# Kernel optimization log

Measured on AMD Instinct MI355X. Metric: run time of the kernel, lower is better.

## Reference

```python
import jax, jax.numpy as jnp
import numpy as np

S = 30000      # num sessions (= num clicks)
ND = 300000    # num displayed rows (10 per session)
F = 64         # f_dim
I = 500        # item_size (news_cnt_short)
PW = 10        # pw_dim
BAND = 20      # pw_band_size
H = 256        # mlp hidden


def setup_inputs() -> dict:
    key = jax.random.key(0)
    ks = jax.random.split(key, 8)
    per = ND // S  # disp rows per session
    disp_sec = jnp.repeat(jnp.arange(S, dtype=jnp.int64), per)          # sorted, every segment nonempty
    click_sub = jnp.arange(S, dtype=jnp.int64) * per                     # one clicked disp row per session
    # banded lower-triangular cumulative-sum indices: row r attends to cols r-0..r-(BAND-1) (clipped at 0)
    rows = jnp.repeat(jnp.arange(S, dtype=jnp.int64), BAND)
    offs = jnp.tile(jnp.arange(BAND, dtype=jnp.int64), S)
    cols = jnp.clip(rows - offs, 0)
    tril_idx = jnp.stack([rows, cols], axis=1)                            # [NT,2]
    click_items = jax.random.randint(ks[0], (S,), 0, I, dtype=jnp.int64)
    disp_items = jax.random.randint(ks[1], (ND,), 0, I, dtype=jnp.int64)
    return {
        'disp_current_feature': jax.random.normal(ks[2], (ND, F), dtype=jnp.float32),
        'Xs_clicked': jax.random.normal(ks[3], (S, F), dtype=jnp.float32),
        'W1': jax.random.normal(ks[4], (F * PW + F, H), dtype=jnp.float32) * 0.05,
        'b1': jnp.zeros((H,), jnp.float32),
        'W2': jax.random.normal(ks[5], (H, H), dtype=jnp.float32) * 0.05,
        'b2': jnp.zeros((H,), jnp.float32),
        'W3': jax.random.normal(ks[6], (H, 1), dtype=jnp.float32) * 0.05,
        'b3': jnp.zeros((1,), jnp.float32),
        'cumsum_tril_indices': tril_idx,
        'cumsum_tril_value_indices': offs,
        'disp_2d_split_sec_ind': disp_sec,
        'click_2d_subindex': click_sub,
        'click_indices': jnp.stack([jnp.arange(S, dtype=jnp.int64), click_items], axis=1),
        'disp_indices': jnp.stack([disp_sec, disp_items], axis=1),
        'section_length': S,
        'item_size': I,
        'pw_dim': PW,
        'band_size': BAND,
    }


def reference(disp_current_feature, Xs_clicked, W1, b1, W2, b2, W3, b3,
              cumsum_tril_indices, cumsum_tril_value_indices,
              disp_2d_split_sec_ind, click_2d_subindex,
              click_indices, disp_indices,
              section_length, item_size, pw_dim, band_size):
    # position weights (fixed 1e-4 as in original forward), gathered per sparse entry
    position_weight = jnp.full((band_size,), 1e-4, dtype=jnp.float32)
    vals = position_weight[cumsum_tril_value_indices]                     # [NT]
    # sparse [S,S] matmul with Xs_clicked expressed as gather + segment_sum (same math as dense matmul)
    contrib = vals[:, None] * Xs_clicked[cumsum_tril_indices[:, 1]]       # [NT,F]
    hist = jax.ops.segment_sum(contrib, cumsum_tril_indices[:, 0], num_segments=section_length)  # [S,F]
    # the pw_dim copies are identical (same position_weight each loop iteration)
    concat_history = jnp.concatenate([hist] * pw_dim, axis=1)             # [S, PW*F]
    disp_hist = concat_history[disp_2d_split_sec_ind]                     # [ND, PW*F]
    feats = jnp.concatenate([disp_hist, disp_current_feature], axis=1)    # [ND, (PW+1)*F]
    h = jax.nn.elu(feats @ W1 + b1)
    h = jax.nn.elu(h @ W2 + b2)
    u_disp = h @ W3 + b3                                                  # [ND,1]
    exp_u = jnp.exp(u_disp)
    sum_exp = jax.ops.segment_sum(exp_u, disp_2d_split_sec_ind, num_segments=section_length)  # [S,1]
    sum_click_u = u_disp[click_2d_subindex]                               # [S,1]
    loss_sum = jnp.sum(-sum_click_u + jnp.log(sum_exp + 1.0))
    click_tensor = jnp.zeros((section_length, item_size), jnp.float32).at[
        click_indices[:, 0], click_indices[:, 1]].add(1.0)
    event_cnt = jnp.sum(click_tensor)
    loss = loss_sum / event_cnt
    dense_exp = jnp.zeros((section_length, item_size), jnp.float32).at[
        disp_indices[:, 0], disp_indices[:, 1]].add(exp_u[:, 0])
    argmax_click = jnp.argmax(click_tensor, axis=1)
    argmax_disp = jnp.argmax(dense_exp, axis=1)
    top2 = jax.lax.top_k(dense_exp, 2)[1]                                 # [S,2]
    p1_sum = jnp.sum(argmax_click == argmax_disp)
    p2_sum = jnp.sum(argmax_click[:, None] == top2)
    precision_1 = p1_sum / event_cnt
    precision_2 = p2_sum / event_cnt
    return (loss, precision_1, precision_2, loss_sum, p1_sum, p2_sum, event_cnt)
```

## Files before the change

kernel.cpp:

```cpp
#include <hip/hip_runtime.h>
#include <hip/hip_bf16.h>

#define TPB 256

typedef _Float16 f16;
typedef f16 f16x8 __attribute__((ext_vector_type(8)));
typedef f16 f16x4 __attribute__((ext_vector_type(4)));
typedef f16 f16x2 __attribute__((ext_vector_type(2)));
typedef float f32x16 __attribute__((ext_vector_type(16)));
typedef unsigned int uint;

union F16x8U { f16x8 v; uint4 q; };
union F16x4U { f16x4 v; uint2 q; };

__device__ __forceinline__ float elu_f(float z) {
    return z > 0.f ? z : __expf(z) - 1.f;
}

__global__ void prepw0_kernel(const float* __restrict__ W1, int PW,
                              f16* __restrict__ W1sT_hi) {
    int t = blockIdx.x * blockDim.x + threadIdx.x;
    if (t < 16384) {
        int n = t >> 6, k = t & 63;
        float s = 0.f;
        for (int p = 0; p < PW; ++p) s += W1[(size_t)(p * 64 + k) * 256 + n];
        W1sT_hi[t] = (f16)s;
    }
}

__global__ __launch_bounds__(TPB, 2) void hist_ahist_kernel(
    const float* __restrict__ Xs, const int* __restrict__ tril,
    const f16* __restrict__ W1sT_hi, const float* __restrict__ b1,
    f16* __restrict__ Ah16, int S, int band,
    const float* __restrict__ W1, const float* __restrict__ W2, int PW,
    f16* __restrict__ W1bT_hi, f16* __restrict__ W2sw,
    int HB)
{
    __shared__ float wA[147 * 68];
    __shared__ f16  hB[128 * 72];

    const int tid = threadIdx.x;

    if ((int)blockIdx.x >= HB) {
        int t = (blockIdx.x - HB) * TPB + tid;
        if (t < 16384) {
            int n = t >> 6, k = t & 63;
            W1bT_hi[t] = (f16)W1[(size_t)(PW * 64 + k) * 256 + n];
        } else {
            int t2 = t - 16384;
            int e  = t2 & 7;
            int n  = (t2 >> 3) & 255;
            int kh = t2 >> 11;
            int k  = (kh >> 1) * 16 + (kh & 1) * 8 + e;
            W2sw[t2] = (f16)W2[(size_t)k * 256 + n];
        }
        return;
    }

    const int SB = blockIdx.x * 128;
    const int base = SB >= 19 ? SB - 19 : 0;

    for (int i = tid; i < 147 * 16; i += TPB) {
        int row = i >> 4, q = i & 15;
        int src = base + row; if (src > S - 1) src = S - 1;
        float4 v = *(const float4*)&Xs[(size_t)src * 64 + q * 4];
        *(float4*)&wA[row * 68 + q * 4] = v;
    }
    __syncthreads();

    const int f = tid & 63, w = tid >> 6;
    for (int k = 0; k < 32; ++k) {
        int rl = w * 32 + k;
        int rg = SB + rl; if (rg > S - 1) rg = S - 1;
        const int* tre = tril + (size_t)rg * band * 2;
        float acc = 0.f;
        for (int o = 0; o < band; ++o) {
            int c = tre[o * 2 + 1] - base;
            c = c < 0 ? 0 : (c > 146 ? 146 : c);
            acc += wA[c * 68 + f];
        }
        hB[rl * 72 + f] = (f16)(acc * 1e-4f);
    }
    __syncthreads();

    const int l = tid & 63, lr = l & 31, hh = l >> 5;
    const int nt0 = 2 * w;

    #pragma unroll
    for (int st = 0; st < 4; ++st) {
        int sgl = st * 32 + lr;
        F16x8U Bh[4];
        #pragma unroll
        for (int ks = 0; ks < 4; ++ks)
            Bh[ks].q = *(const uint4*)&hB[sgl * 72 + ks * 16 + 8 * hh];
        int sg = SB + sgl;
        #pragma unroll
        for (int jn = 0; jn < 2; ++jn) {
            int nt = nt0 + jn;
            f32x16 acc;
            #pragma unroll
            for (int rq = 0; rq < 4; ++rq) {
                float4 bq = *(const float4*)&b1[nt * 32 + rq * 8 + 4 * hh];
                acc[rq * 4 + 0] = bq.x; acc[rq * 4 + 1] = bq.y;
                acc[rq * 4 + 2] = bq.z; acc[rq * 4 + 3] = bq.w;
            }
            const f16* ah = W1sT_hi + (size_t)(nt * 32 + lr) * 64 + 8 * hh;
            #pragma unroll
            for (int ks = 0; ks < 4; ++ks) {
                f16x8 Ah = *(const f16x8*)(ah + ks * 16);
                acc = __builtin_amdgcn_mfma_f32_32x32x16_f16(Ah, Bh[ks].v, acc, 0, 0, 0);
            }
            if (sg < S) {
                F16x8U o0, o1;
                #pragma unroll
                for (int i = 0; i < 8; ++i) {
                    o0.v[i] = (f16)acc[i];
                    o1.v[i] = (f16)acc[8 + i];
                }
                f16* op = Ah16 + (((size_t)sg * 8 + nt) * 2 + hh) * 16;
                *(uint4*)op = o0.q;
                *(uint4*)(op + 8) = o1.q;
            }
        }
    }
}

__global__ __launch_bounds__(512, 4) void mlp14_kernel(
    const float* __restrict__ dispF, const f16* __restrict__ Ah16,
    const f16* __restrict__ W1bT_hi,
    const f16* __restrict__ W2sw,
    const float* __restrict__ b2, const float* __restrict__ W3,
    const float* __restrict__ b3, float* __restrict__ u,
    int ND, int per, float inv_per)
{
    __shared__ uint4 frag[4][16][64];
    f16* dstage = (f16*)&frag[3][0][0];

    const int tid = threadIdx.x;
    const int w = tid >> 6, l = tid & 63, lr = l & 31, hh = l >> 5;
    const int RB = blockIdx.x * 128;
    const int nt = w;

    #pragma unroll
    for (int r = 0; r < 4; ++r) {
        int i = r * 512 + tid;
        int row = i >> 4, q = i & 15;
        int k8 = q >> 1;
        int rg = RB + row; if (rg > ND - 1) rg = ND - 1;
        float4 v = *(const float4*)&dispF[(size_t)rg * 64 + q * 4];
        F16x4U o;
        o.v[0] = (f16)v.x; o.v[1] = (f16)v.y; o.v[2] = (f16)v.z; o.v[3] = (f16)v.w;
        *(uint2*)&dstage[(size_t)(((row >> 5) * 8 + k8) * 256)
                         + ((row & 31) ^ k8) * 8 + (q & 1) * 4] = o.q;
    }

    const f16* a1h = W1bT_hi + (size_t)(nt * 32 + lr) * 64 + 8 * hh;
    f16x8 A1h[4];
    #pragma unroll
    for (int ks = 0; ks < 4; ++ks) A1h[ks] = *(const f16x8*)(a1h + ks * 16);

    const f16* w2p = W2sw + (size_t)hh * 2048 + (size_t)(nt * 32 + lr) * 8;
    f16x8 W2p[4];
    #pragma unroll
    for (int kp = 0; kp < 4; ++kp) W2p[kp] = *(const f16x8*)(w2p + (size_t)kp * 4096);

    int srow[4];
    #pragma unroll
    for (int st = 0; st < 4; ++st) {
        int rg = RB + st * 32 + lr;
        int rgc = rg <= ND - 1 ? rg : ND - 1;
        int sr = (int)((float)rgc * inv_per);
        sr += ((sr + 1) * per <= rgc) ? 1 : 0;
        srow[st] = sr;
    }

    __syncthreads();

    f16x8 Db[2][4];
    uint4 AhP[2][2];
    #pragma unroll
    for (int b = 0; b < 2; ++b) {
        #pragma unroll
        for (int ks = 0; ks < 4; ++ks) {
            int k8 = ks * 2 + hh;
            Db[b][ks] = *(const f16x8*)&dstage[(size_t)((b * 8 + k8) * 256) + (lr ^ k8) * 8];
        }
        const f16* ap = Ah16 + (((size_t)srow[b] * 8 + nt) * 2 + hh) * 16;
        AhP[b][0] = *(const uint4*)ap;
        AhP[b][1] = *(const uint4*)(ap + 8);
    }

    #pragma unroll
    for (int st = 0; st < 4; ++st) {
        f32x16 acc;
        {
            F16x8U u0, u1; u0.q = AhP[st & 1][0]; u1.q = AhP[st & 1][1];
            #pragma unroll
            for (int i = 0; i < 8; ++i) {
                acc[i] = (float)u0.v[i];
                acc[8 + i] = (float)u1.v[i];
            }
        }
        if (st + 2 < 4) {
            const f16* ap = Ah16 + (((size_t)srow[st + 2] * 8 + nt) * 2 + hh) * 16;
            AhP[st & 1][0] = *(const uint4*)ap;
            AhP[st & 1][1] = *(const uint4*)(ap + 8);
        }
        #pragma unroll
        for (int ks = 0; ks < 4; ++ks) {
            acc = __builtin_amdgcn_mfma_f32_32x32x16_f16(A1h[ks], Db[st & 1][ks], acc, 0, 0, 0);
        }
        if (st + 2 < 4) {
            #pragma unroll
            for (int ks = 0; ks < 4; ++ks) {
                int k8 = ks * 2 + hh;
                Db[st & 1][ks] = *(const f16x8*)&dstage[
                    (size_t)(((st + 2) * 8 + k8) * 256) + (lr ^ k8) * 8];
            }
        }

        uint p[4][2];
        #pragma unroll
        for (int rq = 0; rq < 4; ++rq) {
            #pragma unroll
            for (int jj = 0; jj < 2; ++jj) {
                float a = elu_f(acc[rq * 4 + 2 * jj]);
                float b = elu_f(acc[rq * 4 + 2 * jj + 1]);
                f16x2 hp; hp[0] = (f16)a; hp[1] = (f16)b;
                p[rq][jj] = __builtin_bit_cast(uint, hp);
            }
        }
        #pragma unroll
        for (int c = 0; c < 2; ++c) {
            uint s0 = hh ? p[2 * c][0] : p[2 * c + 1][0];
            uint s1 = hh ? p[2 * c][1] : p[2 * c + 1][1];
            uint r0 = __shfl_xor(s0, 32, 64);
            uint r1 = __shfl_xor(s1, 32, 64);
            uint4 B;
            B.x = hh ? r0 : p[2 * c][0];
            B.y = hh ? r1 : p[2 * c][1];
            B.z = hh ? p[2 * c + 1][0] : r0;
            B.w = hh ? p[2 * c + 1][1] : r1;
            frag[st][2 * nt + c][l] = B;
        }
        if (st == 1) __syncthreads();
    }
    __syncthreads();

    f32x16 acc2[4];
    #pragma unroll
    for (int rq = 0; rq < 4; ++rq) {
        float4 bq = *(const float4*)&b2[nt * 32 + rq * 8 + 4 * hh];
        #pragma unroll
        for (int st = 0; st < 4; ++st) {
            acc2[st][rq * 4 + 0] = bq.x; acc2[st][rq * 4 + 1] = bq.y;
            acc2[st][rq * 4 + 2] = bq.z; acc2[st][rq * 4 + 3] = bq.w;
        }
    }

    #pragma unroll
    for (int kt = 0; kt < 16; ++kt) {
        f16x8 Ah = W2p[kt & 3];
        if (kt + 4 < 16) W2p[kt & 3] = *(const f16x8*)(w2p + (size_t)(kt + 4) * 4096);
        #pragma unroll
        for (int st = 0; st < 4; ++st) {
            F16x8U B; B.q = frag[st][kt][l];
            acc2[st] = __builtin_amdgcn_mfma_f32_32x32x16_f16(Ah, B.v, acc2[st], 0, 0, 0);
        }
    }

    float up[4] = {0.f, 0.f, 0.f, 0.f};
    #pragma unroll
    for (int rq = 0; rq < 4; ++rq) {
        float4 wq = *(const float4*)&W3[nt * 32 + rq * 8 + 4 * hh];
        #pragma unroll
        for (int st = 0; st < 4; ++st) {
            up[st] += elu_f(acc2[st][rq * 4 + 0]) * wq.x
                    + elu_f(acc2[st][rq * 4 + 1]) * wq.y
                    + elu_f(acc2[st][rq * 4 + 2]) * wq.z
                    + elu_f(acc2[st][rq * 4 + 3]) * wq.w;
        }
    }
    #pragma unroll
    for (int st = 0; st < 4; ++st) up[st] += __shfl_xor(up[st], 32, 64);

    __syncthreads();
    float* pb = (float*)frag;
    if (hh == 0) {
        #pragma unroll
        for (int st = 0; st < 4; ++st) pb[(w * 4 + st) * 32 + lr] = up[st];
    }
    __syncthreads();
    if (tid < 128) {
        int st = tid >> 5, lrr = tid & 31;
        float v = 0.f;
        #pragma unroll
        for (int w2 = 0; w2 < 8; ++w2) v += pb[(w2 * 4 + st) * 32 + lrr];
        int rg = RB + tid;
        if (rg < ND) u[rg] = v + b3[0];
    }
}

template <int PER>
__global__ void session_kernel(const float* __restrict__ u, const int* __restrict__ clickSub,
                               const int* __restrict__ clickIdx, const int* __restrict__ dispIdx,
                               float* __restrict__ pLoss, int* __restrict__ pP1,
                               int* __restrict__ pP2, int S) {
    int s = blockIdx.x * 64 + threadIdx.x;
    float lossv = 0.f; int p1 = 0, p2 = 0;
    if (s < S) {
        int base = s * PER;
        float ev[PER]; int it[PER];
        float sum_exp = 0.f;
        #pragma unroll
        for (int i = 0; i < PER; ++i) {
            float uu = u[base + i];
            ev[i] = expf(uu);
            sum_exp += ev[i];
            it[i] = dispIdx[(size_t)(base + i) * 2 + 1];
        }
        int crow = clickSub[s];
        lossv = -u[crow] + logf(sum_exp + 1.f);

        float bestv = -1.f; int besti = 0x7FFFFFFF;
        float secv = -1.f;  int seci = 0x7FFFFFFF;
        int ndist = 0;
        #pragma unroll
        for (int i = 0; i < PER; ++i) {
            bool first = true; float tot = 0.f;
            #pragma unroll
            for (int j = 0; j < PER; ++j) {
                if (it[j] == it[i]) { tot += ev[j]; if (j < i) first = false; }
            }
            if (first) {
                ndist++;
                if (tot > bestv || (tot == bestv && it[i] < besti)) {
                    secv = bestv; seci = besti;
                    bestv = tot;  besti = it[i];
                } else if (tot > secv || (tot == secv && it[i] < seci)) {
                    secv = tot; seci = it[i];
                }
            }
        }
        if (ndist < 2) seci = (besti == 0) ? 1 : 0;
        int citem = clickIdx[s * 2 + 1];
        p1 = (citem == besti) ? 1 : 0;
        p2 = (citem == besti || citem == seci) ? 1 : 0;
    }
    #pragma unroll
    for (int off = 32; off > 0; off >>= 1) {
        lossv += __shfl_xor(lossv, off, 64);
        p1 += __shfl_xor(p1, off, 64);
        p2 += __shfl_xor(p2, off, 64);
    }
    if (threadIdx.x == 0) {
        pLoss[blockIdx.x] = lossv; pP1[blockIdx.x] = p1; pP2[blockIdx.x] = p2;
    }
}

__global__ void finalize_kernel(const float* __restrict__ pLoss, const int* __restrict__ pP1,
                                const int* __restrict__ pP2, int nb, float event_cnt,
                                float* __restrict__ out) {
    __shared__ float sf[TPB]; __shared__ int s1[TPB]; __shared__ int s2[TPB];
    int t = threadIdx.x;
    float lf = 0.f; int a1 = 0, a2 = 0;
    for (int i = t; i < nb; i += TPB) { lf += pLoss[i]; a1 += pP1[i]; a2 += pP2[i]; }
    sf[t] = lf; s1[t] = a1; s2[t] = a2;
    __syncthreads();
    for (int off = TPB / 2; off > 0; off >>= 1) {
        if (t < off) { sf[t] += sf[t + off]; s1[t] += s1[t + off]; s2[t] += s2[t + off]; }
        __syncthreads();
    }
    if (t == 0) {
        float ls = sf[0];
        float p1 = (float)s1[0];
        float p2 = (float)s2[0];
        out[0] = ls / event_cnt;
        out[1] = p1 / event_cnt;
        out[2] = p2 / event_cnt;
        out[3] = ls;
        out[4] = p1;
        out[5] = p2;
        out[6] = event_cnt;
    }
}

extern "C" void kernel_launch(void* const* d_in, const int* in_sizes, int n_in,
                              void* d_out, int out_size, void* d_ws, size_t ws_size,
                              hipStream_t stream) {
    const float* dispF    = (const float*)d_in[0];
    const float* Xs       = (const float*)d_in[1];
    const float* W1       = (const float*)d_in[2];
    const float* b1       = (const float*)d_in[3];
    const float* W2       = (const float*)d_in[4];
    const float* b2       = (const float*)d_in[5];
    const float* W3       = (const float*)d_in[6];
    const float* b3       = (const float*)d_in[7];
    const int*   tril     = (const int*)d_in[8];
    const int*   clickSub = (const int*)d_in[11];
    const int*   clickIdx = (const int*)d_in[12];
    const int*   dispIdx  = (const int*)d_in[13];

    const int S    = in_sizes[11];
    const int ND   = in_sizes[10];
    const int F    = in_sizes[1] / S;
    const int H    = in_sizes[3];
    const int NT   = in_sizes[9];
    const int BAND = NT / S;
    const int PW   = in_sizes[2] / (F * H) - 1;
    const int per  = ND / S;

    const int nblk = (ND + 127) / 128;
    const int HB   = (S + 127) / 128;

    float* ws    = (float*)d_ws;
    float* u     = ws;
    const int nb5 = (S + 63) / 64;
    float* pLoss = u + ((size_t)ND + 128);
    int*   pP1   = (int*)(pLoss + nb5);
    int*   pP2   = pP1 + nb5;
    size_t f32_used = (size_t)(pP2 + nb5 - (int*)ws);
    f32_used = (f32_used + 3) & ~(size_t)3;
    f16* W1bT_hi = (f16*)(ws + f32_used);
    f16* W1sT_hi = W1bT_hi + 16384;
    f16* W2sw    = W1sT_hi + 16384;
    f16* Ah16    = W2sw + 65536;

    prepw0_kernel<<<64, TPB, 0, stream>>>(W1, PW, W1sT_hi);
    hist_ahist_kernel<<<HB + 320, TPB, 0, stream>>>(
        Xs, tril, W1sT_hi, b1, Ah16, S, BAND,
        W1, W2, PW, W1bT_hi, W2sw, HB);
    mlp14_kernel<<<nblk, 512, 0, stream>>>(
        dispF, Ah16, W1bT_hi, W2sw, b2, W3, b3, u,
        ND, per, 1.0f / (float)per);
    session_kernel<10><<<nb5, 64, 0, stream>>>(u, clickSub, clickIdx, dispIdx, pLoss, pP1, pP2, S);
    finalize_kernel<<<1, TPB, 0, stream>>>(pLoss, pP1, pP2, nb5, (float)S, (float*)d_out);
}
```

Measured before the change: 143.1 us.

## Split W2 MFMA into two halves, coalesce weight prep writes, vectorize session loads

The layer-2 MFMA loop now processes two sub-tiles at a time in a non-unrolled loop with two accumulators instead of four. This cuts accumulator register pressure, and W2 prefetch wraps around for the second half. Weight-prep kernels now iterate with n fastest so the fp32 W1/W2 reads are coalesced, while the f16 stores become strided. The session kernel loads u and dispIdx with float2/int4 vector loads. The trade-off is serialized MFMA halves with less interleaving, plus reloading W2 fragments for the second half.

```diff
diff --git a/kernel.cpp b/kernel.cpp
--- a/kernel.cpp
+++ b/kernel.cpp
@@ -21,10 +21,10 @@
                               f16* __restrict__ W1sT_hi) {
     int t = blockIdx.x * blockDim.x + threadIdx.x;
     if (t < 16384) {
-        int n = t >> 6, k = t & 63;
+        int k = t >> 8, n = t & 255;
         float s = 0.f;
         for (int p = 0; p < PW; ++p) s += W1[(size_t)(p * 64 + k) * 256 + n];
-        W1sT_hi[t] = (f16)s;
+        W1sT_hi[n * 64 + k] = (f16)s;
     }
 }
 
@@ -44,15 +44,12 @@
     if ((int)blockIdx.x >= HB) {
         int t = (blockIdx.x - HB) * TPB + tid;
         if (t < 16384) {
-            int n = t >> 6, k = t & 63;
-            W1bT_hi[t] = (f16)W1[(size_t)(PW * 64 + k) * 256 + n];
+            int k = t >> 8, n = t & 255;
+            W1bT_hi[n * 64 + k] = (f16)W1[(size_t)(PW * 64 + k) * 256 + n];
         } else {
             int t2 = t - 16384;
-            int e  = t2 & 7;
-            int n  = (t2 >> 3) & 255;
-            int kh = t2 >> 11;
-            int k  = (kh >> 1) * 16 + (kh & 1) * 8 + e;
-            W2sw[t2] = (f16)W2[(size_t)k * 256 + n];
+            int k = t2 >> 8, n = t2 & 255;
+            W2sw[(size_t)(k >> 3) * 2048 + n * 8 + (k & 7)] = (f16)W2[(size_t)k * 256 + n];
         }
         return;
     }
@@ -125,7 +122,7 @@
     }
 }
 
-__global__ __launch_bounds__(512, 4) void mlp14_kernel(
+__global__ __launch_bounds__(512, 4) void mlp15_kernel(
     const float* __restrict__ dispF, const f16* __restrict__ Ah16,
     const f16* __restrict__ W1bT_hi,
     const f16* __restrict__ W2sw,
@@ -247,40 +244,47 @@
     }
     __syncthreads();
 
-    f32x16 acc2[4];
-    #pragma unroll
-    for (int rq = 0; rq < 4; ++rq) {
-        float4 bq = *(const float4*)&b2[nt * 32 + rq * 8 + 4 * hh];
-        #pragma unroll
-        for (int st = 0; st < 4; ++st) {
-            acc2[st][rq * 4 + 0] = bq.x; acc2[st][rq * 4 + 1] = bq.y;
-            acc2[st][rq * 4 + 2] = bq.z; acc2[st][rq * 4 + 3] = bq.w;
-        }
-    }
-
-    #pragma unroll
-    for (int kt = 0; kt < 16; ++kt) {
-        f16x8 Ah = W2p[kt & 3];
-        if (kt + 4 < 16) W2p[kt & 3] = *(const f16x8*)(w2p + (size_t)(kt + 4) * 4096);
-        #pragma unroll
-        for (int st = 0; st < 4; ++st) {
-            F16x8U B; B.q = frag[st][kt][l];
-            acc2[st] = __builtin_amdgcn_mfma_f32_32x32x16_f16(Ah, B.v, acc2[st], 0, 0, 0);
-        }
-    }
-
-    float up[4] = {0.f, 0.f, 0.f, 0.f};
-    #pragma unroll
-    for (int rq = 0; rq < 4; ++rq) {
-        float4 wq = *(const float4*)&W3[nt * 32 + rq * 8 + 4 * hh];
-        #pragma unroll
-        for (int st = 0; st < 4; ++st) {
-            up[st] += elu_f(acc2[st][rq * 4 + 0]) * wq.x
-                    + elu_f(acc2[st][rq * 4 + 1]) * wq.y
-                    + elu_f(acc2[st][rq * 4 + 2]) * wq.z
-                    + elu_f(acc2[st][rq * 4 + 3]) * wq.w;
-        }
-    }
+    float4 bq2 = *(const float4*)&b2[nt * 32 + 0 * 8 + 4 * hh];
+    float up[4];
+
+    #pragma unroll 1
+    for (int half = 0; half < 2; ++half) {
+        const int s0i = 2 * half, s1i = 2 * half + 1;
+        f32x16 accA, accB;
+        #pragma unroll
+        for (int rq = 0; rq < 4; ++rq) {
+            float4 bq = *(const float4*)&b2[nt * 32 + rq * 8 + 4 * hh];
+            accA[rq * 4 + 0] = bq.x; accA[rq * 4 + 1] = bq.y;
+            accA[rq * 4 + 2] = bq.z; accA[rq * 4 + 3] = bq.w;
+            accB[rq * 4 + 0] = bq.x; accB[rq * 4 + 1] = bq.y;
+            accB[rq * 4 + 2] = bq.z; accB[rq * 4 + 3] = bq.w;
+        }
+        #pragma unroll
+        for (int kt = 0; kt < 16; ++kt) {
+            f16x8 Ah = W2p[kt & 3];
+            if (kt + 4 < 16) {
+                W2p[kt & 3] = *(const f16x8*)(w2p + (size_t)(kt + 4) * 4096);
+            } else if (half == 0) {
+                W2p[kt & 3] = *(const f16x8*)(w2p + (size_t)(kt - 12) * 4096);
+            }
+            F16x8U BA; BA.q = frag[s0i][kt][l];
+            F16x8U BB; BB.q = frag[s1i][kt][l];
+            accA = __builtin_amdgcn_mfma_f32_32x32x16_f16(Ah, BA.v, accA, 0, 0, 0);
+            accB = __builtin_amdgcn_mfma_f32_32x32x16_f16(Ah, BB.v, accB, 0, 0, 0);
+        }
+        float uA = 0.f, uB = 0.f;
+        #pragma unroll
+        for (int rq = 0; rq < 4; ++rq) {
+            float4 wq = *(const float4*)&W3[nt * 32 + rq * 8 + 4 * hh];
+            uA += elu_f(accA[rq * 4 + 0]) * wq.x + elu_f(accA[rq * 4 + 1]) * wq.y
+                + elu_f(accA[rq * 4 + 2]) * wq.z + elu_f(accA[rq * 4 + 3]) * wq.w;
+            uB += elu_f(accB[rq * 4 + 0]) * wq.x + elu_f(accB[rq * 4 + 1]) * wq.y
+                + elu_f(accB[rq * 4 + 2]) * wq.z + elu_f(accB[rq * 4 + 3]) * wq.w;
+        }
+        up[s0i] = uA; up[s1i] = uB;
+    }
+    (void)bq2;
+
     #pragma unroll
     for (int st = 0; st < 4; ++st) up[st] += __shfl_xor(up[st], 32, 64);
 
@@ -309,15 +313,22 @@
     int s = blockIdx.x * 64 + threadIdx.x;
     float lossv = 0.f; int p1 = 0, p2 = 0;
     if (s < S) {
-        int base = s * PER;
         float ev[PER]; int it[PER];
+        const float2* up2 = (const float2*)(u + (size_t)s * PER);
+        const int4* dp4 = (const int4*)(dispIdx + (size_t)s * PER * 2);
+        float uu[PER];
+        #pragma unroll
+        for (int j = 0; j < PER / 2; ++j) {
+            float2 v = up2[j];
+            uu[2 * j] = v.x; uu[2 * j + 1] = v.y;
+            int4 d = dp4[j];
+            it[2 * j] = d.y; it[2 * j + 1] = d.w;
+        }
         float sum_exp = 0.f;
         #pragma unroll
         for (int i = 0; i < PER; ++i) {
-            float uu = u[base + i];
-            ev[i] = expf(uu);
+            ev[i] = expf(uu[i]);
             sum_exp += ev[i];
-            it[i] = dispIdx[(size_t)(base + i) * 2 + 1];
         }
         int crow = clickSub[s];
         lossv = -u[crow] + logf(sum_exp + 1.f);
@@ -430,7 +441,7 @@
     hist_ahist_kernel<<<HB + 320, TPB, 0, stream>>>(
         Xs, tril, W1sT_hi, b1, Ah16, S, BAND,
         W1, W2, PW, W1bT_hi, W2sw, HB);
-    mlp14_kernel<<<nblk, 512, 0, stream>>>(
+    mlp15_kernel<<<nblk, 512, 0, stream>>>(
         dispF, Ah16, W1bT_hi, W2sw, b2, W3, b3, u,
         ND, per, 1.0f / (float)per);
     session_kernel<10><<<nb5, 64, 0, stream>>>(u, clickSub, clickIdx, dispIdx, pLoss, pP1, pP2, S);
```

New measurement: 257.5 us. 79.9% more time.
